# Optimization experiments

Measured on AMD Instinct MI355X. Metric: run time of the kernel, lower is better.

Reference implementation:

```python
import jax, jax.numpy as jnp
import numpy as np


def setup_inputs() -> dict:
    key = jax.random.key(0)
    k1, k2 = jax.random.split(key)
    sat = jax.random.normal(k1, (96, 4, 64, 16), dtype=jnp.float32)
    grd = jax.random.normal(k2, (96, 4, 64, 16), dtype=jnp.float32)
    return {"sat_features": sat, "grd_features": grd}


def _corr(sat, grd):
    # sat: [Bs, h, W, c], grd: [Bg, h, Gw, c]
    Bs, h, W, c = sat.shape
    Bg, _, Gw, _ = grd.shape
    # circular pad along the width axis (dim 2), as in the torch code
    sat_pad = jnp.concatenate([sat, sat[:, :, : Gw - 1, :]], axis=2)  # [Bs,h,W+Gw-1,c]
    # torch flips grd along dim 3 (the c axis) before conv2d (cross-correlation)
    kern = grd[:, :, :, ::-1]  # [Bg,h,Gw,c] -> OIHW with O=Bg, I=h, H=Gw, W=c
    out = jax.lax.conv_general_dilated(
        sat_pad, kern, window_strides=(1, 1), padding='VALID',
        dimension_numbers=('NCHW', 'OIHW', 'NCHW'))  # [Bs,Bg,W,1]
    corr = out[..., 0]  # [Bs,Bg,W]
    orien = jnp.argmax(corr, axis=2).astype(jnp.int32)  # [Bs,Bg]
    return corr, orien


def reference(sat_features, grd_features):
    sat, grd = sat_features, grd_features
    Bs, h, W, c = sat.shape
    Bg, _, Gw, _ = grd.shape
    corr, orien = _corr(sat, grd)
    # per-pair circular shift + crop along width
    idx = (jnp.arange(Gw)[None, None, :] + orien[:, :, None]) % W  # [Bs,Bg,Gw]
    i_idx = jnp.arange(Bs)[:, None, None]  # broadcasts with idx
    sat_crop = sat[i_idx, :, idx, :]                # [Bs,Bg,Gw,h,c]
    sat_crop = jnp.transpose(sat_crop, (0, 1, 3, 2, 4))  # [Bs,Bg,h,Gw,c]
    norm = jnp.sqrt(jnp.sum(sat_crop ** 2, axis=(2, 3, 4), keepdims=True) + 1e-8)
    sat_matrix = sat_crop / norm
    dot = jnp.sum(sat_matrix * grd[None], axis=(2, 3, 4))  # [Bs,Bg]
    distance = 2.0 - 2.0 * dot.T                            # [Bg,Bs]
    return (sat_features, grd_features, distance, orien)
```

## Files before the change

kernel.cpp:

```cpp
#include <hip/hip_runtime.h>
#include <math.h>
#include <stdint.h>


#define BS   96
#define H    4
#define W    64
#define C    16
#define BG   96
#define HWC  (H*W*C)

#define SAT_ELEMS (BS*H*W*C)
#define OUT_DIST  (2*SAT_ELEMS)
#define OUT_ORIEN (OUT_DIST + BS*BG)

#define WS_NEEDED ((size_t)2 * SAT_ELEMS * 2)

typedef __attribute__((ext_vector_type(4)))  short short4v;
typedef __attribute__((ext_vector_type(8)))  short short8v;
typedef __attribute__((ext_vector_type(4)))  float f32x4;

__device__ __forceinline__ void bsplit(float x, unsigned short& hi, unsigned short& lo) {
    unsigned int u = __float_as_uint(x);
    unsigned int r = (u + 0x7FFFu + ((u >> 16) & 1u)) >> 16;
    hi = (unsigned short)r;
    float hf = __uint_as_float(r << 16);
    float l = x - hf;
    unsigned int ul = __float_as_uint(l);
    unsigned int rl = (ul + 0x7FFFu + ((ul >> 16) & 1u)) >> 16;
    lo = (unsigned short)rl;
}

__device__ __forceinline__ void glds16(const unsigned short* g, unsigned short* l) {
    __builtin_amdgcn_global_load_lds(
        (const __attribute__((address_space(1))) unsigned int*)g,
        (__attribute__((address_space(3))) unsigned int*)l, 16, 0, 0);
}

__global__ __launch_bounds__(512)
void pf_pack_b(const float* __restrict__ sat, const float* __restrict__ grd,
               unsigned short* __restrict__ Bpk, float* __restrict__ out)
{
    int t = blockIdx.x * 512 + threadIdx.x;
    int lane = t & 63;
    int f    = t >> 6;
    int nt6  = f % 6;
    int g    = f / 6;
    int kh   = g & 1;
    int j    = g >> 1;

    int col = nt6 * 16 + (lane & 15);
    int u   = lane >> 4;
    int h   = kh * 2 + (u >> 1);
    int k0  = (u & 1) * 8;

    const float* row = grd + ((size_t)(col * 4 + h) * 64 + j) * 16 + (8 - k0);
    float tmp[8];
    *(float4*)&tmp[0] = *(const float4*)(row);
    *(float4*)&tmp[4] = *(const float4*)(row + 4);

    short8v hv, lv;
    #pragma unroll
    for (int e = 0; e < 8; ++e) {
        unsigned short hi, lo;
        bsplit(tmp[7 - e], hi, lo);
        hv[e] = (short)hi; lv[e] = (short)lo;
    }
    size_t base = (size_t)f << 10;
    *(short8v*)&Bpk[base + lane * 8]       = hv;
    *(short8v*)&Bpk[base + 512 + lane * 8] = lv;

    const float4* s4 = (const float4*)sat;
    const float4* g4 = (const float4*)grd;
    float4* o4 = (float4*)out;
    #pragma unroll
    for (int idx = t; idx < 2 * SAT_ELEMS / 4; idx += 49152) {
        o4[idx] = (idx < SAT_ELEMS / 4) ? s4[idx] : g4[idx - SAT_ELEMS / 4];
    }
}

#define MFMA16(a, b, c) __builtin_amdgcn_mfma_f32_16x16x32_bf16((a), (b), (c), 0, 0, 0)

__global__ __launch_bounds__(512, 4)
void pf_fused(const float* __restrict__ sat, const float* __restrict__ grd,
              const unsigned short* __restrict__ Bpk, float* __restrict__ out)
{
    __shared__ unsigned short sHi[4096], sLo[4096];
    __shared__ unsigned short Bb[2][4][512];
    __shared__ float corrPart[2][64][17];
    __shared__ float redW[8];
    __shared__ int   orienL[16];

    const int bs  = blockIdx.y;
    const int nt6 = blockIdx.x;
    const int bg0 = nt6 * 16;
    const int tid = threadIdx.x;
    const int wv  = tid >> 6, lane = tid & 63;
    const int u   = lane >> 4, l15 = lane & 15;
    const int m   = wv & 3;
    const int kh  = wv >> 2;

    if (wv < 4) {
        const int kh_ = wv & 1, pl_ = wv >> 1;
        const unsigned short* src =
            Bpk + (((size_t)kh_ * 6 + nt6) << 10) + (pl_ << 9) + lane * 8;
        glds16(src, &Bb[0][wv][0]);
    }

    {
        const float4* satB = (const float4*)(sat + (size_t)bs * HWC);
        float np = 0.f;
        #pragma unroll
        for (int t = tid; t < 1024; t += 512) {
            float4 v = satB[t];
            int e = 4 * t;
            int h = e >> 10, w = (e >> 4) & 63, k = e & 15;
            int cc = (h * 16 + k) >> 3;
            int dst = w * 64 + ((cc ^ (w & 7)) * 8) + (k & 7);
            short4v hvv, lvv;
            unsigned short hi, lo;
            bsplit(v.x, hi, lo); hvv[0] = hi; lvv[0] = lo;
            bsplit(v.y, hi, lo); hvv[1] = hi; lvv[1] = lo;
            bsplit(v.z, hi, lo); hvv[2] = hi; lvv[2] = lo;
            bsplit(v.w, hi, lo); hvv[3] = hi; lvv[3] = lo;
            *(short4v*)&sHi[dst] = hvv;
            *(short4v*)&sLo[dst] = lvv;
            np = fmaf(v.x, v.x, fmaf(v.y, v.y, fmaf(v.z, v.z, fmaf(v.w, v.w, np))));
        }
        #pragma unroll
        for (int off = 32; off; off >>= 1) np += __shfl_xor(np, off);
        if (lane == 0) redW[wv] = np;
    }
    __syncthreads();

    f32x4 c0 = {0.f,0.f,0.f,0.f}, c1 = {0.f,0.f,0.f,0.f};
    const int cc = kh * 4 + u;

    int cur = 0;
    for (int j = 0; j < 64; ++j) {
        if (j < 63 && wv < 4) {
            const int kh_ = wv & 1, pl_ = wv >> 1;
            const unsigned short* src =
                Bpk + (((size_t)((j + 1) * 2 + kh_) * 6 + nt6) << 10) + (pl_ << 9) + lane * 8;
            glds16(src, &Bb[cur ^ 1][wv][0]);
        }
        const int r = (m * 16 + l15 + j) & 63;
        const int aoff = (r << 6) + ((cc ^ (r & 7)) << 3);
        short8v ah = *(const short8v*)&sHi[aoff];
        short8v al = *(const short8v*)&sLo[aoff];
        short8v bh = *(const short8v*)&Bb[cur][kh][lane * 8];
        short8v bl = *(const short8v*)&Bb[cur][2 + kh][lane * 8];
        c0 = MFMA16(ah, bh, c0);
        c1 = MFMA16(ah, bl, c1);
        c1 = MFMA16(al, bh, c1);
        c0 = MFMA16(al, bl, c0);
        __syncthreads();
        cur ^= 1;
    }
    f32x4 acc = c0 + c1;

    {
        const int rr = m * 16 + u * 4;
        #pragma unroll
        for (int reg = 0; reg < 4; ++reg)
            corrPart[kh][rr + reg][l15] = acc[reg];
    }
    __syncthreads();

    #pragma unroll
    for (int t = 0; t < 2; ++t) {
        const int bgc = wv * 2 + t;
        float v = corrPart[0][lane][bgc] + corrPart[1][lane][bgc];
        int idx = lane;
        #pragma unroll
        for (int off = 32; off; off >>= 1) {
            float ov = __shfl_xor(v, off);
            int   oi = __shfl_xor(idx, off);
            if (ov > v || (ov == v && oi < idx)) { v = ov; idx = oi; }
        }
        if (lane == 0) {
            orienL[bgc] = idx;
            out[OUT_ORIEN + bs * BG + bg0 + bgc] = (float)idx;
        }
    }
    __syncthreads();

    const float nrm = sqrtf(((redW[0] + redW[1]) + (redW[2] + redW[3]))
                          + ((redW[4] + redW[5]) + (redW[6] + redW[7])) + 1e-8f);

    #pragma unroll
    for (int t = 0; t < 2; ++t) {
        const int bgc = wv * 2 + t;
        const int bg = bg0 + bgc;
        const int r = (lane + orienL[bgc]) & 63;
        float s = 0.f;
        #pragma unroll
        for (int h = 0; h < 4; ++h) {
            const float4* sp = (const float4*)&sat[(((size_t)bs * 4 + h) * 64 + r) * 16];
            const float4* gp = (const float4*)&grd[(((size_t)bg * 4 + h) * 64 + lane) * 16];
            #pragma unroll
            for (int c4 = 0; c4 < 4; ++c4) {
                float4 sv = sp[c4];
                float4 gv = gp[c4];
                s = fmaf(sv.x, gv.x, fmaf(sv.y, gv.y, fmaf(sv.z, gv.z, fmaf(sv.w, gv.w, s))));
            }
        }
        #pragma unroll
        for (int off = 32; off; off >>= 1) s += __shfl_xor(s, off);
        if (lane == 0)
            out[OUT_DIST + (size_t)bg * BS + bs] = 2.f - 2.f * (s / nrm);
    }
}

__device__ __forceinline__ int satIdxFB(int hw, int c4) {
    return hw * 16 + 4 * ((c4 + (hw >> 1)) & 3);
}
__device__ __forceinline__ float rot_add(int baddr, float p) {
    return __int_as_float(__builtin_amdgcn_ds_bpermute(baddr, __float_as_int(p)));
}
__device__ __forceinline__ float dot_rev(const float4 s0, const float4 s1,
                                         const float4 s2, const float4 s3,
                                         const float* __restrict__ g) {
    float p0 = fmaf(s0.x, g[15], fmaf(s0.y, g[14], fmaf(s0.z, g[13], s0.w * g[12])));
    float p1 = fmaf(s1.x, g[11], fmaf(s1.y, g[10], fmaf(s1.z, g[ 9], s1.w * g[ 8])));
    float p2 = fmaf(s2.x, g[ 7], fmaf(s2.y, g[ 6], fmaf(s2.z, g[ 5], s2.w * g[ 4])));
    float p3 = fmaf(s3.x, g[ 3], fmaf(s3.y, g[ 2], fmaf(s3.z, g[ 1], s3.w * g[ 0])));
    return (p0 + p1) + (p2 + p3);
}
#define NB 8
__global__ __launch_bounds__(256)
void pf_fused_fb(const float* __restrict__ sat, const float* __restrict__ grd,
                 float* __restrict__ out)
{
    __shared__ float satL[H * W * C];
    __shared__ float partL[NB * 4 * W];
    __shared__ float sumL[4];
    __shared__ float dotP[NB * 4];
    __shared__ int   orienL[NB];
    const int bs = blockIdx.y, bg0 = blockIdx.x * NB;
    const int tid = threadIdx.x, wv = tid >> 6, lane = tid & 63;
    const float4* sp = (const float4*)(sat + (((size_t)bs * H + wv) * W + lane) * C);
    const float4 s0 = sp[0], s1 = sp[1], s2 = sp[2], s3 = sp[3];
    { const int hw = wv * W + lane;
      *(float4*)&satL[satIdxFB(hw,0)] = s0; *(float4*)&satL[satIdxFB(hw,1)] = s1;
      *(float4*)&satL[satIdxFB(hw,2)] = s2; *(float4*)&satL[satIdxFB(hw,3)] = s3; }
    { float a = fmaf(s0.x,s0.x,fmaf(s0.y,s0.y,fmaf(s0.z,s0.z,s0.w*s0.w)));
      float b = fmaf(s1.x,s1.x,fmaf(s1.y,s1.y,fmaf(s1.z,s1.z,s1.w*s1.w)));
      float c = fmaf(s2.x,s2.x,fmaf(s2.y,s2.y,fmaf(s2.z,s2.z,s2.w*s2.w)));
      float d = fmaf(s3.x,s3.x,fmaf(s3.y,s3.y,fmaf(s3.z,s3.z,s3.w*s3.w)));
      float s = (a+b)+(c+d);
      #pragma unroll
      for (int off = 32; off; off >>= 1) s += __shfl_xor(s, off);
      if (lane == 0) sumL[wv] = s; }
    const float* gpB = grd + (size_t)(bg0 * H + wv) * W * C;
    #pragma unroll
    for (int bp = 0; bp < NB/2; ++bp) {
        const float* gA = gpB + (2*bp) * HWC;
        const float* gB2 = gpB + (2*bp+1) * HWC;
        float accA = 0.f, accB = 0.f;
        int baddr = lane << 2;
        #pragma unroll 2
        for (int j = 0; j < W; ++j) {
            float pA = dot_rev(s0,s1,s2,s3, gA + j*C);
            float pB = dot_rev(s0,s1,s2,s3, gB2 + j*C);
            accA += rot_add(baddr, pA); accB += rot_add(baddr, pB);
            baddr = (baddr + 4) & 255;
        }
        partL[((2*bp)*4 + wv)*W + lane] = accA;
        partL[((2*bp+1)*4 + wv)*W + lane] = accB;
    }
    __syncthreads();
    for (int b = wv; b < NB; b += 4) {
        float v = (partL[(b*4+0)*W+lane] + partL[(b*4+1)*W+lane])
                + (partL[(b*4+2)*W+lane] + partL[(b*4+3)*W+lane]);
        int idx = lane;
        #pragma unroll
        for (int off = 32; off; off >>= 1) {
            float ov = __shfl_xor(v, off); int oi = __shfl_xor(idx, off);
            if (ov > v || (ov == v && oi < idx)) { v = ov; idx = oi; }
        }
        if (lane == 0) { orienL[b] = idx; out[OUT_ORIEN + bs*BG + (bg0+b)] = (float)idx; }
    }
    __syncthreads();
    const float nrm = sqrtf(sumL[0]+sumL[1]+sumL[2]+sumL[3] + 1e-8f);
    { float dp[NB];
      #pragma unroll
      for (int b = 0; b < NB; ++b) {
          const int row = (lane + orienL[b]) & 63;
          const float* gRow = grd + (((size_t)(bg0+b)*H + wv)*W + lane)*C;
          float s = 0.f;
          #pragma unroll
          for (int c4 = 0; c4 < 4; ++c4) {
              float4 sv = *(const float4*)&satL[satIdxFB(wv*W+row, c4)];
              float4 gv = *(const float4*)(gRow + 4*c4);
              s = fmaf(sv.x,gv.x, fmaf(sv.y,gv.y, fmaf(sv.z,gv.z, fmaf(sv.w,gv.w, s))));
          }
          dp[b] = s;
      }
      #pragma unroll
      for (int b = 0; b < NB; ++b) {
          float s = dp[b];
          #pragma unroll
          for (int off = 32; off; off >>= 1) s += __shfl_xor(s, off);
          if (lane == 0) dotP[b*4 + wv] = s;
      } }
    __syncthreads();
    if (tid < NB) {
        float d = ((dotP[tid*4+0]+dotP[tid*4+1])+(dotP[tid*4+2]+dotP[tid*4+3])) / nrm;
        out[OUT_DIST + (size_t)(bg0+tid)*BS + bs] = 2.f - 2.f*d;
    }
}

extern "C" void kernel_launch(void* const* d_in, const int* in_sizes, int n_in,
                              void* d_out, int out_size, void* d_ws, size_t ws_size,
                              hipStream_t stream) {
    const float* sat = (const float*)d_in[0];
    const float* grd = (const float*)d_in[1];
    float* out = (float*)d_out;

    if (ws_size < WS_NEEDED) {
        hipMemcpyAsync(out,             sat, (size_t)SAT_ELEMS * sizeof(float),
                       hipMemcpyDeviceToDevice, stream);
        hipMemcpyAsync(out + SAT_ELEMS, grd, (size_t)SAT_ELEMS * sizeof(float),
                       hipMemcpyDeviceToDevice, stream);
        dim3 grid(BG / NB, BS);
        pf_fused_fb<<<grid, 256, 0, stream>>>(sat, grd, out);
        return;
    }

    unsigned short* Bpk = (unsigned short*)d_ws;
    pf_pack_b<<<96, 512, 0, stream>>>(sat, grd, Bpk, out);
    pf_fused<<<dim3(6, BS), 512, 0, stream>>>(sat, grd, Bpk, out);
}
```

Baseline: 58.90 us.

## Batch four j-steps per barrier and reduce corr partials in place

The B-operand staging buffer now holds four j-steps per stage, and all eight waves share the async loads. This cuts the per-iteration __syncthreads from 64 to 16 and unrolls four MFMA groups between barriers. The two k-half partial correlations are now summed into one shared array in two phases instead of being stored separately. This adds one extra barrier and grows LDS use for the B buffer, which may limit occupancy.

```diff
diff --git a/kernel.cpp b/kernel.cpp
--- a/kernel.cpp
+++ b/kernel.cpp
@@ -86,8 +86,8 @@
               const unsigned short* __restrict__ Bpk, float* __restrict__ out)
 {
     __shared__ unsigned short sHi[4096], sLo[4096];
-    __shared__ unsigned short Bb[2][4][512];
-    __shared__ float corrPart[2][64][17];
+    __shared__ unsigned short Bb[2][4][2][2][512];
+    __shared__ float corrS[64][17];
     __shared__ float redW[8];
     __shared__ int   orienL[16];
 
@@ -97,15 +97,17 @@
     const int tid = threadIdx.x;
     const int wv  = tid >> 6, lane = tid & 63;
     const int u   = lane >> 4, l15 = lane & 15;
-    const int m   = wv & 3;
+    const int mt  = wv & 3;
     const int kh  = wv >> 2;
 
-    if (wv < 4) {
-        const int kh_ = wv & 1, pl_ = wv >> 1;
-        const unsigned short* src =
-            Bpk + (((size_t)kh_ * 6 + nt6) << 10) + (pl_ << 9) + lane * 8;
-        glds16(src, &Bb[0][wv][0]);
-    }
+    #define ISSUE(buf_, j0_, c_) { \
+        const int jl_ = (c_) >> 2, kh_ = ((c_) >> 1) & 1, pl_ = (c_) & 1; \
+        const unsigned short* src_ = Bpk \
+            + (((size_t)(((j0_) + jl_) * 2 + kh_) * 6 + nt6) << 10) + (pl_ << 9) + lane * 8; \
+        glds16(src_, &Bb[buf_][jl_][kh_][pl_][0]); }
+
+    ISSUE(0, 0, 2 * wv);
+    ISSUE(0, 0, 2 * wv + 1);
 
     {
         const float4* satB = (const float4*)(sat + (size_t)bs * HWC);
@@ -134,43 +136,53 @@
     __syncthreads();
 
     f32x4 c0 = {0.f,0.f,0.f,0.f}, c1 = {0.f,0.f,0.f,0.f};
-    const int cc = kh * 4 + u;
-
+    const int mbase = mt * 16 + l15;
+    const int ccA = kh * 4 + u;
     int cur = 0;
-    for (int j = 0; j < 64; ++j) {
-        if (j < 63 && wv < 4) {
-            const int kh_ = wv & 1, pl_ = wv >> 1;
-            const unsigned short* src =
-                Bpk + (((size_t)((j + 1) * 2 + kh_) * 6 + nt6) << 10) + (pl_ << 9) + lane * 8;
-            glds16(src, &Bb[cur ^ 1][wv][0]);
-        }
-        const int r = (m * 16 + l15 + j) & 63;
-        const int aoff = (r << 6) + ((cc ^ (r & 7)) << 3);
-        short8v ah = *(const short8v*)&sHi[aoff];
-        short8v al = *(const short8v*)&sLo[aoff];
-        short8v bh = *(const short8v*)&Bb[cur][kh][lane * 8];
-        short8v bl = *(const short8v*)&Bb[cur][2 + kh][lane * 8];
-        c0 = MFMA16(ah, bh, c0);
-        c1 = MFMA16(ah, bl, c1);
-        c1 = MFMA16(al, bh, c1);
-        c0 = MFMA16(al, bl, c0);
+
+    for (int bt = 0; bt < 16; ++bt) {
+        if (bt < 15) {
+            const int j0n = (bt + 1) * 4;
+            ISSUE(cur ^ 1, j0n, 2 * wv);
+            ISSUE(cur ^ 1, j0n, 2 * wv + 1);
+        }
+        #pragma unroll
+        for (int jl = 0; jl < 4; ++jl) {
+            const int j = bt * 4 + jl;
+            const int r = (mbase + j) & 63;
+            const int aoff = (r << 6) + ((ccA ^ (r & 7)) << 3);
+            short8v ah = *(const short8v*)&sHi[aoff];
+            short8v al = *(const short8v*)&sLo[aoff];
+            short8v bh = *(const short8v*)&Bb[cur][jl][kh][0][lane * 8];
+            short8v bl = *(const short8v*)&Bb[cur][jl][kh][1][lane * 8];
+            c0 = MFMA16(ah, bh, c0);
+            c1 = MFMA16(ah, bl, c1);
+            c1 = MFMA16(al, bh, c1);
+            c0 = MFMA16(al, bl, c0);
+        }
         __syncthreads();
         cur ^= 1;
     }
+    #undef ISSUE
     f32x4 acc = c0 + c1;
 
-    {
-        const int rr = m * 16 + u * 4;
+    if (kh == 0) {
         #pragma unroll
         for (int reg = 0; reg < 4; ++reg)
-            corrPart[kh][rr + reg][l15] = acc[reg];
+            corrS[mt * 16 + u * 4 + reg][l15] = acc[reg];
+    }
+    __syncthreads();
+    if (kh == 1) {
+        #pragma unroll
+        for (int reg = 0; reg < 4; ++reg)
+            corrS[mt * 16 + u * 4 + reg][l15] += acc[reg];
     }
     __syncthreads();
 
     #pragma unroll
     for (int t = 0; t < 2; ++t) {
         const int bgc = wv * 2 + t;
-        float v = corrPart[0][lane][bgc] + corrPart[1][lane][bgc];
+        float v = corrS[lane][bgc];
         int idx = lane;
         #pragma unroll
         for (int off = 32; off; off >>= 1) {
```

Result: no change. 57.98 us (-1.6%).
